# Performance work log

Hardware: AMD Instinct MI355X
Metric: run time of the kernel (lower is better)

The kernel has to match this reference:

```python
import jax, jax.numpy as jnp
import numpy as np

# ---- static config (mirrors GaussianLSS __init__) ----
ORF_H, ORF_W = 256, 704
FC, FH, FW = 128, 32, 88
D_ST, D_END, D_STEP = 4.0, 45.0, 1.0
OUT_C = 128
ERROR_TOL = 1.0
OPACITY_THR = 0.05
XB = (-50.0, 50.0, 1.0)
YB = (-50.0, 50.0, 1.0)
BEV_H = int(round((YB[1] - YB[0]) / YB[2]))
BEV_W = int(round((XB[1] - XB[0]) / XB[2]))
DS = np.arange(D_ST, D_END, D_STEP, dtype=np.float32)
D = DS.shape[0]  # 41
BN_EPS = 1e-3
CHUNK = 512      # gaussians composited per scan step (16896 = 33*512)
B, NCAM = 1, 6


def make_frustum():
    ds = jnp.broadcast_to(jnp.asarray(DS)[:, None, None], (D, FH, FW))
    xs = jnp.broadcast_to(jnp.linspace(0.0, ORF_W - 1.0, FW)[None, None, :], (D, FH, FW))
    ys = jnp.broadcast_to(jnp.linspace(0.0, ORF_H - 1.0, FH)[None, :, None], (D, FH, FW))
    return jnp.stack([xs, ys, ds], -1)  # [D,FH,FW,3]


def get_geometry(rots, trans, intrins, post_rots, post_trans):
    fr = make_frustum()
    pts = fr[None, None] - post_trans[:, :, None, None, None, :]
    pts = jnp.einsum('bnij,bndhwj->bndhwi', jnp.linalg.inv(post_rots), pts)
    pts = jnp.concatenate([pts[..., :2] * pts[..., 2:3], pts[..., 2:3]], -1)
    comb = jnp.einsum('bnij,bnjk->bnik', rots, jnp.linalg.inv(intrins))
    pts = jnp.einsum('bnij,bndhwj->bndhwi', comb, pts) + trans[:, :, None, None, None, :]
    return pts  # [B,N,D,FH,FW,3] ego-frame frustum points


def conv2d(x, w, b, pad):
    y = jax.lax.conv_general_dilated(x, w, (1, 1), [(pad, pad), (pad, pad)],
                                     dimension_numbers=('NCHW', 'OIHW', 'NCHW'))
    return y + b[None, :, None, None]


def bnorm(x, g, bt, m, v):
    s = (g / jnp.sqrt(v + BN_EPS))[None, :, None, None]
    return (x - m[None, :, None, None]) * s + bt[None, :, None, None]


def splat(means, cov6, colors, ops, valid_in):
    # Differentiable BEV gaussian rasterization (3DGS math, orthographic BEV camera,
    # all depths equal -> compositing in stable gaussian-index order).
    H, W = BEV_H, BEV_W
    sh, sw = H / 2.0, W / 2.0  # h/h_meters with FoV=2 (BEVCamera)
    my = -sh * means[:, 1] + H / 2.0  # pixel row (full_proj_transform row 0)
    mx = -sw * means[:, 0] + W / 2.0  # pixel col (row 1)
    a = sh * sh * cov6[:, 3] + 0.3    # 2D cov = J Sigma_xy J^T, +0.3 low-pass as in 3DGS
    c = sw * sw * cov6[:, 0] + 0.3
    b = sh * sw * cov6[:, 1]
    det = a * c - b * b
    valid = valid_in & (det > 0)
    inv_det = jnp.where(det > 0, 1.0 / det, 0.0)
    cA, cB, cC = c * inv_det, -b * inv_det, a * inv_det
    pi = jnp.repeat(jnp.arange(H, dtype=jnp.float32), W)  # [P] pixel rows
    pj = jnp.tile(jnp.arange(W, dtype=jnp.float32), H)    # [P] pixel cols
    G = means.shape[0]
    nchunk = G // CHUNK
    resh = lambda x: x.reshape((nchunk, CHUNK) + x.shape[1:])
    chunks = (resh(my), resh(mx), resh(cA), resh(cB), resh(cC),
              resh(ops), resh(valid), resh(colors))

    def body(carry, ch):
        logT, acc = carry
        my_c, mx_c, A, Bc, Cc, op_c, val_c, col_c = ch
        dI = pi[None, :] - my_c[:, None]                     # [Gc,P]
        dJ = pj[None, :] - mx_c[:, None]
        q = A[:, None] * dI * dI + 2.0 * Bc[:, None] * dI * dJ + Cc[:, None] * dJ * dJ
        alpha = jnp.minimum(0.99, op_c[:, None] * jnp.exp(-0.5 * q))
        alpha = jnp.where(val_c[:, None] & (q >= 0) & (alpha >= 1.0 / 255.0), alpha, 0.0)
        log1m = jnp.log1p(-alpha)
        cum = jnp.cumsum(log1m, axis=0)
        T = jnp.exp(logT[None, :] + cum - log1m)             # transmittance before each gaussian
        acc = acc + jnp.einsum('gp,gc->pc', alpha * T, col_c)
        return (logT + cum[-1], acc), None

    P = H * W
    init = (jnp.zeros((P,), jnp.float32), jnp.zeros((P, colors.shape[1]), jnp.float32))
    (_, acc), _ = jax.lax.scan(jax.checkpoint(body), init, chunks)
    return acc.reshape(H, W, -1).transpose(2, 0, 1)  # [C,H,W], bg is zeros


def _forward(cam2ego_rot, cam2ego_trans, cam_intrins, post_cam2ego_rot, post_cam2ego_trans,
             img_feats, conv1_w, conv1_b, bn1_g, bn1_b, bn1_m, bn1_v,
             conv2_w, conv2_b, bn2_g, bn2_b, bn2_m, bn2_v, conv3_w, conv3_b):
    geom = get_geometry(cam2ego_rot, cam2ego_trans, cam_intrins, post_cam2ego_rot, post_cam2ego_trans)
    b, n = img_feats.shape[:2]
    x = img_feats.reshape(b * n, FC, FH, FW)
    x = jax.nn.relu(bnorm(conv2d(x, conv1_w, conv1_b, 1), bn1_g, bn1_b, bn1_m, bn1_v))
    x = jax.nn.relu(bnorm(conv2d(x, conv2_w, conv2_b, 1), bn2_g, bn2_b, bn2_m, bn2_v))
    x = conv2d(x, conv3_w, conv3_b, 0)
    depth_prob = jax.nn.softmax(x[:, :D], axis=1).reshape(b, n, D, FH, FW)
    opac = jax.nn.sigmoid(x[:, D:D + 1]).reshape(b, n, FH, FW)
    feats = x[:, D + 1:].reshape(b, n, OUT_C, FH, FW)
    # per-pixel gaussian moments of the depth distribution (compute_gaussian)
    means = jnp.einsum('bndhw,bndhwi->bnhwi', depth_prob, geom)
    delta = means[:, :, None] - geom                                       # [B,N,D,FH,FW,3]
    cov = jnp.einsum('bndhw,bndhwi,bndhwj->bnhwij', depth_prob, delta, delta) * (ERROR_TOL ** 2 / 9.0)
    center = jnp.array([(XB[0] + XB[1]) / 2.0, (YB[0] + YB[1]) / 2.0, 0.0], jnp.float32)
    scale = jnp.array([2.0 / (XB[1] - XB[0]), 2.0 / (YB[1] - YB[0]), 1.0], jnp.float32)
    m_n = (means - center) * scale
    cov_n = cov * (scale[:, None] * scale[None, :])
    cov6 = jnp.stack([cov_n[..., 0, 0], cov_n[..., 0, 1], cov_n[..., 0, 2],
                      cov_n[..., 1, 1], cov_n[..., 1, 2], cov_n[..., 2, 2]], -1)
    g = n * FH * FW
    colors = feats.transpose(0, 1, 3, 4, 2).reshape(b, g, OUT_C)
    m_n = m_n.reshape(b, g, 3)
    cov6 = cov6.reshape(b, g, 6)
    ops = opac.reshape(b, g)
    mask = ops > OPACITY_THR  # opacity filtering == zero contribution, order preserved
    bev = jax.vmap(splat)(m_n, cov6, colors, ops, mask)                    # [B,C,H,W]
    num_gaussians = mask.astype(jnp.float32).sum(-1).mean()
    return bev, num_gaussians


def setup_inputs():
    key = jax.random.key(0)
    ks = jax.random.split(key, 8)
    # camera-to-ego rotations: cam->ego axis permutation composed with per-camera yaw
    yaw = np.linspace(0.0, 2.0 * np.pi, NCAM, endpoint=False).astype(np.float32)
    cz, sz = np.cos(yaw), np.sin(yaw)
    rotz = np.zeros((NCAM, 3, 3), np.float32)
    rotz[:, 0, 0] = cz; rotz[:, 0, 1] = -sz
    rotz[:, 1, 0] = sz; rotz[:, 1, 1] = cz
    rotz[:, 2, 2] = 1.0
    perm = np.array([[0.0, 0.0, 1.0], [-1.0, 0.0, 0.0], [0.0, -1.0, 0.0]], np.float32)
    rots = np.einsum('nij,jk->nik', rotz, perm)
    cam2ego_rot = jnp.asarray(np.broadcast_to(rots, (B, NCAM, 3, 3)).copy())
    cam2ego_trans = jax.random.normal(ks[0], (B, NCAM, 3), jnp.float32)
    K = np.array([[600.0, 0.0, ORF_W / 2.0], [0.0, 600.0, ORF_H / 2.0], [0.0, 0.0, 1.0]], np.float32)
    cam_intrins = jnp.asarray(np.broadcast_to(K, (B, NCAM, 3, 3)).copy())
    post_cam2ego_rot = jnp.broadcast_to(jnp.eye(3, dtype=jnp.float32), (B, NCAM, 3, 3)) + jnp.zeros((B, NCAM, 3, 3), jnp.float32)
    post_cam2ego_trans = jnp.zeros((B, NCAM, 3), jnp.float32)
    img_feats = jax.random.normal(ks[1], (B, NCAM, FC, FH, FW), jnp.float32)
    def conv_init(k, o, i, kh, kw):
        return jax.random.normal(k, (o, i, kh, kw), jnp.float32) * (1.0 / np.sqrt(i * kh * kw))
    return dict(cam2ego_rot=cam2ego_rot, cam2ego_trans=cam2ego_trans, cam_intrins=cam_intrins,
                post_cam2ego_rot=post_cam2ego_rot, post_cam2ego_trans=post_cam2ego_trans,
                img_feats=img_feats,
                conv1_w=conv_init(ks[2], FC, FC, 3, 3), conv1_b=jnp.zeros((FC,), jnp.float32),
                bn1_g=jnp.ones((FC,), jnp.float32), bn1_b=jnp.zeros((FC,), jnp.float32),
                bn1_m=jnp.zeros((FC,), jnp.float32), bn1_v=jnp.ones((FC,), jnp.float32),
                conv2_w=conv_init(ks[3], FC, FC, 3, 3), conv2_b=jnp.zeros((FC,), jnp.float32),
                bn2_g=jnp.ones((FC,), jnp.float32), bn2_b=jnp.zeros((FC,), jnp.float32),
                bn2_m=jnp.zeros((FC,), jnp.float32), bn2_v=jnp.ones((FC,), jnp.float32),
                conv3_w=conv_init(ks[4], OUT_C + D + 1, FC, 1, 1),
                conv3_b=jax.random.normal(ks[5], (OUT_C + D + 1,), jnp.float32) * 0.1)


def reference(cam2ego_rot, cam2ego_trans, cam_intrins, post_cam2ego_rot, post_cam2ego_trans,
              img_feats, conv1_w, conv1_b, bn1_g, bn1_b, bn1_m, bn1_v,
              conv2_w, conv2_b, bn2_g, bn2_b, bn2_m, bn2_v, conv3_w, conv3_b):
    return _forward(cam2ego_rot, cam2ego_trans, cam_intrins, post_cam2ego_rot, post_cam2ego_trans,
                    img_feats, conv1_w, conv1_b, bn1_g, bn1_b, bn1_m, bn1_v,
                    conv2_w, conv2_b, bn2_g, bn2_b, bn2_m, bn2_v, conv3_w, conv3_b)
```

## Files before the change

### kernel.cpp

```cpp
#include <hip/hip_runtime.h>

#define NCAM 6
#define FC   128
#define FH_  32
#define FW_  88
#define NPIX (FH_*FW_)
#define PH   34
#define PW   92
#define PPIX (PH*PW)
#define ND   41
#define X3D  42
#define OUTC 128
#define GTOT (NCAM*NPIX)
#define BEVH 100
#define BEVW 100
#define NPXB (BEVH*BEVW)
#define NTILE 25
#define NWORD 264
#define NMASKW (NTILE*NTILE*NWORD)
#define WCAP  70000
#define CSIZE 64
#define CBLK  2048

#define SZA     (NCAM*FC*PPIX)
#define WS_CAM  0
#define WS_A    256
#define WS_RB   (WS_A  + SZA)
#define WS_X3   (WS_RB + SZA)
#define WS_GS   (WS_X3 + NCAM*X3D*NPIX)
#define WS_WL   (WS_GS + GTOT*8)
#define WS_BASE (WS_WL + WCAP)

__device__ inline void inv3x3(const float* m, float* o) {
    float a=m[0],b=m[1],c=m[2],d=m[3],e=m[4],f=m[5],g=m[6],h=m[7],i=m[8];
    float A=e*i-f*h, B=c*h-b*i, C=b*f-c*e;
    float Dd=f*g-d*i, E=a*i-c*g, F=c*d-a*f;
    float Gg=d*h-e*g, H=b*g-a*h, I=a*e-b*d;
    float r = 1.0f/(a*A + b*Dd + c*Gg);
    o[0]=A*r; o[1]=B*r; o[2]=C*r; o[3]=Dd*r; o[4]=E*r; o[5]=F*r;
    o[6]=Gg*r; o[7]=H*r; o[8]=I*r;
}

__global__ __launch_bounds__(256) void pad_input_kernel(const float* __restrict__ src,
        float* __restrict__ dst, float* __restrict__ rb,
        float* __restrict__ outp, unsigned long long* __restrict__ masks) {
    int idx = blockIdx.x*256 + threadIdx.x;
    if (idx < NMASKW) masks[idx] = 0ull;
    if (idx <= NPXB*OUTC) outp[idx] = 0.0f;
    if (idx >= NCAM*FC*PPIX) return;
    int plane = idx / PPIX, pp = idx - plane*PPIX;
    int y = pp / PW, x = pp - y*PW;
    bool interior = (y >= 1 && y <= FH_ && x >= 1 && x <= FW_);
    float v = 0.0f;
    if (interior)
        v = src[(size_t)plane*NPIX + (y-1)*FW_ + (x-1)];
    dst[idx] = v;
    if (!interior) rb[idx] = 0.0f;
}

__global__ __launch_bounds__(128) void conv3x3_pf_kernel(
        const float* __restrict__ in, float* __restrict__ out, const float* __restrict__ w,
        const float* __restrict__ cb, const float* __restrict__ bg, const float* __restrict__ bb,
        const float* __restrict__ bm, const float* __restrict__ bv) {
    const int n   = blockIdx.x;
    const int co0 = blockIdx.y * 4;
    const int qid = blockIdx.z * 128 + threadIdx.x;
    if (qid >= 704) return;
    const int y = qid / 22, x0 = (qid - y*22) * 4;
    float scale[4], shift[4];
    #pragma unroll
    for (int c=0;c<4;c++) {
        float s = bg[co0+c] * rsqrtf(bv[co0+c] + 1e-3f);
        scale[c] = s;
        shift[c] = (cb[co0+c] - bm[co0+c]) * s + bb[co0+c];
    }
    float acc[4][4] = {};
    const float* ip = in + (size_t)n*FC*PPIX + y*PW + x0;
    const float* wb = w + (size_t)co0*FC*9;
    float4 p4[3]; float2 p2[3];
    #pragma unroll
    for (int r=0;r<3;r++) {
        p4[r] = *(const float4*)(ip + r*PW);
        p2[r] = *(const float2*)(ip + r*PW + 4);
    }
    for (int ci=0; ci<FC; ++ci) {
        float v[3][6];
        #pragma unroll
        for (int r=0;r<3;r++) {
            v[r][0]=p4[r].x; v[r][1]=p4[r].y; v[r][2]=p4[r].z; v[r][3]=p4[r].w;
            v[r][4]=p2[r].x; v[r][5]=p2[r].y;
        }
        if (ci + 1 < FC) {
            const float* ipn = ip + PPIX;
            #pragma unroll
            for (int r=0;r<3;r++) {
                p4[r] = *(const float4*)(ipn + r*PW);
                p2[r] = *(const float2*)(ipn + r*PW + 4);
            }
        }
        #pragma unroll
        for (int c=0;c<4;c++) {
            const float* wr = wb + (size_t)c*FC*9 + ci*9;
            float w00=wr[0],w01=wr[1],w02=wr[2],w10=wr[3],w11=wr[4],
                  w12=wr[5],w20=wr[6],w21=wr[7],w22=wr[8];
            #pragma unroll
            for (int p=0;p<4;p++) {
                float a = acc[c][p];
                a = fmaf(w00, v[0][p], a); a = fmaf(w01, v[0][p+1], a); a = fmaf(w02, v[0][p+2], a);
                a = fmaf(w10, v[1][p], a); a = fmaf(w11, v[1][p+1], a); a = fmaf(w12, v[1][p+2], a);
                a = fmaf(w20, v[2][p], a); a = fmaf(w21, v[2][p+1], a); a = fmaf(w22, v[2][p+2], a);
                acc[c][p] = a;
            }
        }
        ip += PPIX;
    }
    const int po = (y+1)*PW + (x0+1);
    #pragma unroll
    for (int c=0;c<4;c++) {
        float* op = out + ((size_t)n*FC + co0 + c)*PPIX + po;
        #pragma unroll
        for (int p=0;p<4;p++)
            op[p] = fmaxf(fmaf(acc[c][p], scale[c], shift[c]), 0.0f);
    }
}

__global__ __launch_bounds__(256) void conv1x1_kernel(const float* __restrict__ in,
        float* __restrict__ x3d, float* __restrict__ colors,
        const float* __restrict__ w, const float* __restrict__ b) {
    const int n   = blockIdx.x;
    const int px  = blockIdx.y * 256 + threadIdx.x;
    const int co0 = blockIdx.z * 8;
    const int y   = px / FW_, x = px - y*FW_;
    const int pp  = (y+1)*PW + (x+1);
    const float* wr[8];
    float acc[8];
    #pragma unroll
    for (int k=0;k<8;k++) {
        int co = min(co0 + k, 169);
        wr[k]  = w + (size_t)co*FC;
        acc[k] = b[co];
    }
    const float* ip = in + (size_t)n*FC*PPIX + pp;
    #pragma unroll 4
    for (int ci=0; ci<FC; ++ci) {
        float v = ip[(size_t)ci*PPIX];
        #pragma unroll
        for (int k=0;k<8;k++) acc[k] = fmaf(wr[k][ci], v, acc[k]);
    }
    #pragma unroll
    for (int k=0;k<8;k++) {
        int co = co0 + k;
        if (co < X3D)
            x3d[((size_t)n*X3D + co)*NPIX + px] = acc[k];
        else if (co < 170)
            colors[(((size_t)(n*NPIX + px)) << 7) + (co - X3D)] = acc[k];
    }
}

__global__ __launch_bounds__(256) void moments_masks_kernel(const float* __restrict__ x3,
        const float* __restrict__ rot, const float* __restrict__ tr,
        const float* __restrict__ intr, const float* __restrict__ prot,
        const float* __restrict__ ptr_, float* __restrict__ gauss,
        unsigned long long* __restrict__ masks, float* __restrict__ ng) {
    __shared__ float cc[24];
    const int n = blockIdx.x / 11;
    if (threadIdx.x == 0) {
        float M1[9], Ki[9];
        inv3x3(prot + n*9, M1);
        inv3x3(intr + n*9, Ki);
        const float* R = rot + n*9;
        #pragma unroll
        for (int i=0;i<9;i++) cc[i] = M1[i];
        #pragma unroll
        for (int i=0;i<3;i++) cc[9+i] = ptr_[n*3+i];
        #pragma unroll
        for (int i=0;i<3;i++)
            #pragma unroll
            for (int j=0;j<3;j++)
                cc[12+i*3+j] = R[i*3+0]*Ki[0+j] + R[i*3+1]*Ki[3+j] + R[i*3+2]*Ki[6+j];
        #pragma unroll
        for (int i=0;i<3;i++) cc[21+i] = tr[n*3+i];
    }
    __syncthreads();
    const int gi = blockIdx.x*256 + threadIdx.x;
    const int p  = gi - n*NPIX;
    const int h  = p / FW_, xp = p - h*FW_;
    float u = xp * (703.0f/87.0f);
    float v = h  * (255.0f/31.0f);
    float fx = u - cc[9], fy = v - cc[10], fz = -cc[11];
    float p0x = cc[0]*fx + cc[1]*fy + cc[2]*fz;
    float p0y = cc[3]*fx + cc[4]*fy + cc[5]*fz;
    float p0z = cc[6]*fx + cc[7]*fy + cc[8]*fz;
    const float* lg = x3 + (size_t)n*X3D*NPIX + p;

    float lgv[ND];
    #pragma unroll
    for (int d=0; d<ND; ++d) lgv[d] = lg[(size_t)d*NPIX];

    float mxl = -1e30f;
    #pragma unroll
    for (int d=0; d<ND; ++d) mxl = fmaxf(mxl, lgv[d]);

    float s=0.f, sgx=0.f, sgy=0.f;
    #pragma unroll
    for (int d=0; d<ND; ++d) {
        float e  = __expf(lgv[d] - mxl);
        lgv[d] = e;
        float dz = 4.0f + (float)d;
        float pz = p0z + dz*cc[8];
        float px = (p0x + dz*cc[2]) * pz;
        float py = (p0y + dz*cc[5]) * pz;
        float gx = cc[12]*px + cc[13]*py + cc[14]*pz + cc[21];
        float gy = cc[15]*px + cc[16]*py + cc[17]*pz + cc[22];
        s += e; sgx += e*gx; sgy += e*gy;
    }
    float inv_s = 1.0f/s;
    float mex = sgx*inv_s, mey = sgy*inv_s;
    float cxx=0.f, cxy=0.f, cyy=0.f;
    #pragma unroll
    for (int d=0; d<ND; ++d) {
        float e  = lgv[d];
        float dz = 4.0f + (float)d;
        float pz = p0z + dz*cc[8];
        float px = (p0x + dz*cc[2]) * pz;
        float py = (p0y + dz*cc[5]) * pz;
        float gx = cc[12]*px + cc[13]*py + cc[14]*pz + cc[21];
        float gy = cc[15]*px + cc[16]*py + cc[17]*pz + cc[22];
        float dxv = gx - mex, dyv = gy - mey;
        cxx += e*dxv*dxv; cxy += e*dxv*dyv; cyy += e*dyv*dyv;
    }
    const float k9 = inv_s * (1.0f/9.0f);
    cxx *= k9; cxy *= k9; cyy *= k9;

    float lo = lg[(size_t)ND*NPIX];
    float op = 1.0f/(1.0f + __expf(-lo));
    bool mask = op > 0.05f;

    const float SC = 0.02f, SH = 50.0f, SW = 50.0f;
    float my = -SH*(mey*SC) + 50.0f;
    float mx = -SW*(mex*SC) + 50.0f;
    float a  = SH*SH*(cyy*SC*SC) + 0.3f;
    float b  = SH*SW*(cxy*SC*SC);
    float c  = SW*SW*(cxx*SC*SC) + 0.3f;
    float det = a*c - b*b;
    bool valid = mask && (det > 0.0f);
    float A, B2, C, qm, ri, rj;
    if (valid) {
        float idet = 1.0f/det;
        A = c*idet; B2 = -2.0f*b*idet; C = a*idet;
        qm = 2.0f*__logf(255.0f*op);
        ri = sqrtf(qm*a); rj = sqrtf(qm*c);
    } else { A=B2=C=0.f; qm=-1.0f; ri=-1e30f; rj=-1e30f; }
    float* gp = gauss + (size_t)gi*8;
    gp[0]=my; gp[1]=mx; gp[2]=A; gp[3]=B2; gp[4]=C; gp[5]=qm; gp[6]=ri; gp[7]=rj;

    unsigned long long bal = __ballot(mask);
    if ((threadIdx.x & 63) == 0) atomicAdd(ng, (float)__popcll(bal));

    if (!valid) return;
    const float B = 0.5f*B2;
    const float invC = 1.0f / C;
    const float k2 = C*A - B*B;
    int ti0 = max(0, (int)floorf((my - ri) * 0.25f));
    int ti1 = min(NTILE-1, (int)floorf((my + ri) * 0.25f));
    const int wi = gi >> 6;
    const unsigned long long bit = 1ull << (gi & 63);
    for (int ti = ti0; ti <= ti1; ++ti) {
        float jmn = 1e30f, jmx = -1e30f;
        #pragma unroll
        for (int r = 0; r < 4; ++r) {
            int i = 4*ti + r;
            if (i < 0 || i > 99) continue;
            float di = (float)i - my;
            float disc = C*qm - k2*di*di;
            if (disc < 0.0f) continue;
            float sd = sqrtf(disc);
            float jc = -B*di;
            jmn = fminf(jmn, (jc - sd)*invC + mx);
            jmx = fmaxf(jmx, (jc + sd)*invC + mx);
        }
        if (jmx < jmn) continue;
        int jl = max(0, (int)ceilf(jmn));
        int jh = min(99, (int)floorf(jmx));
        if (jl > jh) continue;
        for (int tj = (jl >> 2); tj <= (jh >> 2); ++tj)
            atomicOr(&masks[(size_t)(ti*NTILE + tj)*NWORD + wi], bit);
    }
}

__global__ __launch_bounds__(256) void cnt_kernel(const unsigned long long* __restrict__ masks,
                                                  int* __restrict__ cnt) {
    __shared__ int sc;
    const int tile = blockIdx.x, t = threadIdx.x;
    if (t == 0) sc = 0;
    __syncthreads();
    if (t < NWORD) atomicAdd(&sc, __popcll(masks[(size_t)tile*NWORD + t]));
    __syncthreads();
    if (t == 0) cnt[tile] = sc;
}

__global__ __launch_bounds__(640) void scan_kernel(const int* __restrict__ cnt,
        int* __restrict__ off, int* __restrict__ choff, int* __restrict__ nwork) {
    __shared__ int wsum[16], wsum2[16];
    const int t = threadIdx.x;
    const int lane = t & 63, wv = t >> 6;
    int c  = (t < NTILE*NTILE) ? cnt[t] : 0;
    int ch = (c + CSIZE-1) >> 6;
    int v = c, v2 = ch;
    #pragma unroll
    for (int o = 1; o < 64; o <<= 1) {
        int u  = __shfl_up(v,  (unsigned)o, 64);
        int u2 = __shfl_up(v2, (unsigned)o, 64);
        if (lane >= o) { v += u; v2 += u2; }
    }
    if (lane == 63) { wsum[wv] = v; wsum2[wv] = v2; }
    __syncthreads();
    int pre = 0, pre2 = 0;
    for (int w2 = 0; w2 < wv; ++w2) { pre += wsum[w2]; pre2 += wsum2[w2]; }
    int inc = v + pre, inc2 = v2 + pre2;
    if (t < NTILE*NTILE) { off[t] = inc - c; choff[t] = inc2 - ch; }
    if (t == NTILE*NTILE - 1) {
        off[NTILE*NTILE] = inc;
        choff[NTILE*NTILE] = inc2;
        nwork[0] = (inc2 > WCAP) ? WCAP : inc2;
    }
}

__global__ __launch_bounds__(256) void fill_kernel(const unsigned long long* __restrict__ masks,
        const int* __restrict__ cnt, const int* __restrict__ off, const int* __restrict__ choff,
        unsigned short* __restrict__ list, int* __restrict__ wl) {
    __shared__ unsigned long long sw[NWORD];
    __shared__ int wpre[NWORD];
    const int tile = blockIdx.x, t = threadIdx.x;
    if (t < NWORD) sw[t] = masks[(size_t)tile*NWORD + t];
    __syncthreads();
    if (t == 0) {
        int run = 0;
        for (int w2 = 0; w2 < NWORD; ++w2) { wpre[w2] = run; run += __popcll(sw[w2]); }
    }
    __syncthreads();
    if (t < NWORD) {
        unsigned long long m = sw[t];
        int pos = off[tile] + wpre[t], base = t << 6;
        while (m) { int b = __builtin_ctzll(m); m &= m - 1; list[pos++] = (unsigned short)(base + b); }
    }
    int nch = (cnt[tile] + CSIZE-1)/CSIZE;
    int c0 = choff[tile];
    if (t < nch && c0 + t < WCAP) wl[c0 + t] = (tile << 9) | t;
}

__device__ inline float eval_alpha(const float4 g0, const float4 g1, float fi, float fj) {
    float dI = fi - g0.x, dJ = fj - g0.y;
    float q = dI*(g0.z*dI + g0.w*dJ) + g1.x*dJ*dJ;
    if (q < 0.0f || q > g1.y) return 0.0f;
    return fminf(0.99f, 0.003921568627f * __expf(0.5f*(g1.y - q)));
}

__global__ __launch_bounds__(256) void chunk_sums_kernel(const float* __restrict__ gauss,
        const unsigned short* __restrict__ list, const int* __restrict__ cnt,
        const int* __restrict__ off, const int* __restrict__ wl, const int* __restrict__ nwork,
        float* __restrict__ base) {
    const int nw = nwork[0];
    const int lane = threadIdx.x & 63;
    const int wid  = (blockIdx.x * 256 + threadIdx.x) >> 6;
    const int nwv  = (gridDim.x * 256) >> 6;
    const int px = lane & 15, kg = lane >> 4;
    for (int e = wid; e < nw; e += nwv) {
        int v = wl[e], tile = v >> 9, c = v & 511;
        int hbase = off[tile] + (c << 6);
        int nh = min(CSIZE, cnt[tile] - (c << 6));
        const int i0 = (tile / NTILE) * 4, j0 = (tile % NTILE) * 4;
        const float fi = (float)(i0 + (px >> 2)), fj = (float)(j0 + (px & 3));
        float s = 1.0f;
        for (int k = kg; k < nh; k += 4) {
            int g = list[hbase + k];
            float4 g0 = *(const float4*)(gauss + ((size_t)g << 3));
            float4 g1 = *(const float4*)(gauss + ((size_t)g << 3) + 4);
            float a = eval_alpha(g0, g1, fi, fj);
            s *= (1.0f - a);
        }
        s *= __shfl_xor(s, 16, 64);
        s *= __shfl_xor(s, 32, 64);
        if (lane < 16) base[(size_t)e*16 + lane] = s;
    }
}

__global__ __launch_bounds__(256) void chunk_prefix_kernel(const int* __restrict__ choff,
                                                           float* __restrict__ base) {
    __shared__ float part[16][17];
    const int tile = blockIdx.x, t = threadIdx.x;
    const int c0 = choff[tile], nch = choff[tile+1] - c0;
    if (nch == 0) return;
    const int px = t & 15, cg = t >> 4;
    const int L16 = (nch + 15) >> 4;
    const int a0 = cg*L16, a1 = min(nch, a0 + L16);
    float s = 1.0f;
    for (int c = a0; c < a1; ++c) s *= base[(size_t)(c0 + c)*16 + px];
    part[cg][px] = s;
    __syncthreads();
    if (t < 16) {
        float run = 1.0f;
        #pragma unroll
        for (int k = 0; k < 16; ++k) { float tmp = part[k][t]; part[k][t] = run; run *= tmp; }
    }
    __syncthreads();
    float run = part[cg][px];
    for (int c = a0; c < a1; ++c) {
        size_t idx = (size_t)(c0 + c)*16 + px;
        float tmp = base[idx];
        base[idx] = run;
        run *= tmp;
    }
}

__global__ __launch_bounds__(256) void composite_kernel(const float* __restrict__ gauss,
        const float* __restrict__ colors, const unsigned short* __restrict__ list,
        const int* __restrict__ cnt, const int* __restrict__ off, const int* __restrict__ wl,
        const int* __restrict__ nwork, const float* __restrict__ base, float* __restrict__ out) {
    const int nw = nwork[0];
    const int t = threadIdx.x;
    const int lane = t & 63;
    const int e_px = t >> 4, e_kg = t & 15;
    const int a_cs4 = t & 31, a_pxq = t >> 5;
    __shared__ unsigned short slist[2][CSIZE];
    __shared__ float s_w[CSIZE][17];
    const int per = (nw + CBLK - 1) / CBLK;
    int e0 = blockIdx.x * per;
    if (e0 >= nw) return;
    int e1 = min(nw, e0 + per);

    float4 acc0 = make_float4(0.f,0.f,0.f,0.f);
    float4 acc1 = make_float4(0.f,0.f,0.f,0.f);
    int cur_tile = wl[e0] >> 9;
    int cur_i0 = (cur_tile / NTILE) * 4, cur_j0 = (cur_tile % NTILE) * 4;

    int buf = 0;
    {
        int v = wl[e0], tl = v >> 9, c = v & 511;
        int nh0 = min(CSIZE, cnt[tl] - (c << 6));
        if (t < nh0) slist[0][t] = list[off[tl] + (c << 6) + t];
    }

    for (int e = e0; e < e1; ++e) {
        int v = wl[e], tile = v >> 9, c = v & 511;
        if (tile != cur_tile) {
            const int pix0 = (cur_i0 + (a_pxq >> 2)) * BEVW + cur_j0 + (a_pxq & 3);
            const int pix1 = pix0 + 2 * BEVW;
            float* op = out + (size_t)(a_cs4 << 2) * NPXB;
            atomicAdd(op + 0*NPXB + pix0, acc0.x); atomicAdd(op + 1*NPXB + pix0, acc0.y);
            atomicAdd(op + 2*NPXB + pix0, acc0.z); atomicAdd(op + 3*NPXB + pix0, acc0.w);
            atomicAdd(op + 0*NPXB + pix1, acc1.x); atomicAdd(op + 1*NPXB + pix1, acc1.y);
            atomicAdd(op + 2*NPXB + pix1, acc1.z); atomicAdd(op + 3*NPXB + pix1, acc1.w);
            acc0 = make_float4(0.f,0.f,0.f,0.f);
            acc1 = make_float4(0.f,0.f,0.f,0.f);
            cur_tile = tile;
            cur_i0 = (tile / NTILE) * 4; cur_j0 = (tile % NTILE) * 4;
        }
        const int nh = min(CSIZE, cnt[cur_tile] - (c << 6));
        __syncthreads();
        if (e + 1 < e1) {
            int v2 = wl[e+1], tl2 = v2 >> 9, c2 = v2 & 511;
            int nh2 = min(CSIZE, cnt[tl2] - (c2 << 6));
            if (t < nh2) slist[buf^1][t] = list[off[tl2] + (c2 << 6) + t];
        }
        {
            const float fi = (float)(cur_i0 + (e_px >> 2)), fj = (float)(cur_j0 + (e_px & 3));
            const int k0 = e_kg << 2;
            float a4[4]; float p = 1.0f;
            #pragma unroll
            for (int i = 0; i < 4; ++i) {
                int k = k0 + i;
                float a = 0.0f;
                if (k < nh) {
                    int g = slist[buf][k];
                    float4 g0 = *(const float4*)(gauss + ((size_t)g << 3));
                    float4 g1 = *(const float4*)(gauss + ((size_t)g << 3) + 4);
                    a = eval_alpha(g0, g1, fi, fj);
                }
                a4[i] = a;
                p *= (1.0f - a);
            }
            float s = p;
            #pragma unroll
            for (int o = 1; o < 16; o <<= 1) {
                float u = __shfl_up(s, (unsigned)o, 64);
                if ((lane & 15) >= o) s *= u;
            }
            float ex = __shfl_up(s, 1u, 64);
            float T = base[(size_t)e*16 + e_px] * (((lane & 15) == 0) ? 1.0f : ex);
            #pragma unroll
            for (int i = 0; i < 4; ++i) {
                float wv = a4[i] * T; T -= wv;
                s_w[k0 + i][e_px] = wv;
            }
        }
        __syncthreads();
        const float* colbase = colors;
        if (nh == CSIZE) {
            #pragma unroll 8
            for (int k = 0; k < CSIZE; ++k) {
                int g = slist[buf][k];
                float w0 = s_w[k][a_pxq];
                float w1 = s_w[k][a_pxq + 8];
                float4 cl = *(const float4*)(colbase + ((size_t)g << 7) + (a_cs4 << 2));
                acc0.x = fmaf(w0, cl.x, acc0.x); acc0.y = fmaf(w0, cl.y, acc0.y);
                acc0.z = fmaf(w0, cl.z, acc0.z); acc0.w = fmaf(w0, cl.w, acc0.w);
                acc1.x = fmaf(w1, cl.x, acc1.x); acc1.y = fmaf(w1, cl.y, acc1.y);
                acc1.z = fmaf(w1, cl.z, acc1.z); acc1.w = fmaf(w1, cl.w, acc1.w);
            }
        } else {
            #pragma unroll 4
            for (int k = 0; k < nh; ++k) {
                int g = slist[buf][k];
                float w0 = s_w[k][a_pxq];
                float w1 = s_w[k][a_pxq + 8];
                float4 cl = *(const float4*)(colbase + ((size_t)g << 7) + (a_cs4 << 2));
                acc0.x = fmaf(w0, cl.x, acc0.x); acc0.y = fmaf(w0, cl.y, acc0.y);
                acc0.z = fmaf(w0, cl.z, acc0.z); acc0.w = fmaf(w0, cl.w, acc0.w);
                acc1.x = fmaf(w1, cl.x, acc1.x); acc1.y = fmaf(w1, cl.y, acc1.y);
                acc1.z = fmaf(w1, cl.z, acc1.z); acc1.w = fmaf(w1, cl.w, acc1.w);
            }
        }
        buf ^= 1;
    }
    const int pix0 = (cur_i0 + (a_pxq >> 2)) * BEVW + cur_j0 + (a_pxq & 3);
    const int pix1 = pix0 + 2 * BEVW;
    float* op = out + (size_t)(a_cs4 << 2) * NPXB;
    atomicAdd(op + 0*NPXB + pix0, acc0.x); atomicAdd(op + 1*NPXB + pix0, acc0.y);
    atomicAdd(op + 2*NPXB + pix0, acc0.z); atomicAdd(op + 3*NPXB + pix0, acc0.w);
    atomicAdd(op + 0*NPXB + pix1, acc1.x); atomicAdd(op + 1*NPXB + pix1, acc1.y);
    atomicAdd(op + 2*NPXB + pix1, acc1.z); atomicAdd(op + 3*NPXB + pix1, acc1.w);
}

extern "C" void kernel_launch(void* const* d_in, const int* in_sizes, int n_in,
                              void* d_out, int out_size, void* d_ws, size_t ws_size,
                              hipStream_t stream) {
    const float* rot  = (const float*)d_in[0];
    const float* tr   = (const float*)d_in[1];
    const float* intr = (const float*)d_in[2];
    const float* prot = (const float*)d_in[3];
    const float* ptr_ = (const float*)d_in[4];
    const float* img  = (const float*)d_in[5];
    const float* c1w  = (const float*)d_in[6];  const float* c1b = (const float*)d_in[7];
    const float* b1g  = (const float*)d_in[8];  const float* b1b = (const float*)d_in[9];
    const float* b1m  = (const float*)d_in[10]; const float* b1v = (const float*)d_in[11];
    const float* c2w  = (const float*)d_in[12]; const float* c2b = (const float*)d_in[13];
    const float* b2g  = (const float*)d_in[14]; const float* b2b = (const float*)d_in[15];
    const float* b2m  = (const float*)d_in[16]; const float* b2v = (const float*)d_in[17];
    const float* c3w  = (const float*)d_in[18]; const float* c3b = (const float*)d_in[19];
    float* out = (float*)d_out;
    float* ws  = (float*)d_ws;
    float* RA  = ws + WS_A;
    float* RB  = ws + WS_RB;
    float* X3B = ws + WS_X3;
    float* GS  = ws + WS_GS;
    int*   WL  = (int*)(ws + WS_WL);
    float* BASE = ws + WS_BASE;
    unsigned long long* MASKS = (unsigned long long*)BASE;
    int* AUXI = (int*)(ws + WS_X3 + 330000);
    int* CNT = AUXI;
    int* OFF = AUXI + 640;
    int* CHOFF = AUXI + 1280;
    int* NWORK = AUXI + 1920;
    unsigned short* LIST = (unsigned short*)RA;
    float* COL = RB;
    float* ngp = out + (size_t)NPXB*OUTC;

    pad_input_kernel<<<(NCAM*FC*PPIX + 255)/256, 256, 0, stream>>>(img, RA, RB, out, MASKS);
    conv3x3_pf_kernel<<<dim3(NCAM,32,6), 128, 0, stream>>>(RA, RB, c1w, c1b, b1g, b1b, b1m, b1v);
    conv3x3_pf_kernel<<<dim3(NCAM,32,6), 128, 0, stream>>>(RB, RA, c2w, c2b, b2g, b2b, b2m, b2v);
    conv1x1_kernel<<<dim3(NCAM,11,22), 256, 0, stream>>>(RA, X3B, COL, c3w, c3b);
    moments_masks_kernel<<<GTOT/256, 256, 0, stream>>>(X3B, rot, tr, intr, prot, ptr_,
                                                       GS, MASKS, ngp);
    cnt_kernel<<<NTILE*NTILE, 256, 0, stream>>>(MASKS, CNT);
    scan_kernel<<<1, 640, 0, stream>>>(CNT, OFF, CHOFF, NWORK);
    fill_kernel<<<NTILE*NTILE, 256, 0, stream>>>(MASKS, CNT, OFF, CHOFF, LIST, WL);
    chunk_sums_kernel<<<8192, 256, 0, stream>>>(GS, LIST, CNT, OFF, WL, NWORK, BASE);
    chunk_prefix_kernel<<<NTILE*NTILE, 256, 0, stream>>>(CHOFF, BASE);
    composite_kernel<<<CBLK, 256, 0, stream>>>(GS, COL, LIST, CNT, OFF, WL, NWORK, BASE, out);
}
```

Baseline: 473.2 us.

## Split gaussian chunk across wave halves with 4-pixel register tiles in composite

Reassigns composite threads so each handles one channel quad for four pixels of a BEV row, with the two 32-lane halves of each wave taking even and odd gaussians of the chunk. This doubles reuse of each color float4 load across pixels and halves the per-thread loop trip count. A cross-half shuffle reduction before the atomic writes merges the partial sums, so each pixel still gets one atomic per channel. It costs more accumulator registers and adds shuffle work.

```diff
diff --git a/kernel.cpp b/kernel.cpp
--- a/kernel.cpp
+++ b/kernel.cpp
@@ -421,7 +421,9 @@
     const int t = threadIdx.x;
     const int lane = t & 63;
     const int e_px = t >> 4, e_kg = t & 15;
-    const int a_cs4 = t & 31, a_pxq = t >> 5;
+    const int cs4 = t & 31;
+    const int par = (t >> 5) & 1;
+    const int pq  = t >> 6;
     __shared__ unsigned short slist[2][CSIZE];
     __shared__ float s_w[CSIZE][17];
     const int per = (nw + CBLK - 1) / CBLK;
@@ -429,8 +431,9 @@
     if (e0 >= nw) return;
     int e1 = min(nw, e0 + per);
 
-    float4 acc0 = make_float4(0.f,0.f,0.f,0.f);
-    float4 acc1 = make_float4(0.f,0.f,0.f,0.f);
+    float4 acc[4];
+    #pragma unroll
+    for (int j=0;j<4;j++) acc[j] = make_float4(0.f,0.f,0.f,0.f);
     int cur_tile = wl[e0] >> 9;
     int cur_i0 = (cur_tile / NTILE) * 4, cur_j0 = (cur_tile % NTILE) * 4;
 
@@ -444,15 +447,25 @@
     for (int e = e0; e < e1; ++e) {
         int v = wl[e], tile = v >> 9, c = v & 511;
         if (tile != cur_tile) {
-            const int pix0 = (cur_i0 + (a_pxq >> 2)) * BEVW + cur_j0 + (a_pxq & 3);
-            const int pix1 = pix0 + 2 * BEVW;
-            float* op = out + (size_t)(a_cs4 << 2) * NPXB;
-            atomicAdd(op + 0*NPXB + pix0, acc0.x); atomicAdd(op + 1*NPXB + pix0, acc0.y);
-            atomicAdd(op + 2*NPXB + pix0, acc0.z); atomicAdd(op + 3*NPXB + pix0, acc0.w);
-            atomicAdd(op + 0*NPXB + pix1, acc1.x); atomicAdd(op + 1*NPXB + pix1, acc1.y);
-            atomicAdd(op + 2*NPXB + pix1, acc1.z); atomicAdd(op + 3*NPXB + pix1, acc1.w);
-            acc0 = make_float4(0.f,0.f,0.f,0.f);
-            acc1 = make_float4(0.f,0.f,0.f,0.f);
+            #pragma unroll
+            for (int j = 0; j < 4; ++j) {
+                acc[j].x += __shfl_xor(acc[j].x, 32, 64);
+                acc[j].y += __shfl_xor(acc[j].y, 32, 64);
+                acc[j].z += __shfl_xor(acc[j].z, 32, 64);
+                acc[j].w += __shfl_xor(acc[j].w, 32, 64);
+            }
+            if (par == 0) {
+                float* op = out + (size_t)(cs4 << 2) * NPXB + (cur_i0 + pq) * BEVW + cur_j0;
+                #pragma unroll
+                for (int j = 0; j < 4; ++j) {
+                    atomicAdd(op + 0*NPXB + j, acc[j].x);
+                    atomicAdd(op + 1*NPXB + j, acc[j].y);
+                    atomicAdd(op + 2*NPXB + j, acc[j].z);
+                    atomicAdd(op + 3*NPXB + j, acc[j].w);
+                }
+            }
+            #pragma unroll
+            for (int j=0;j<4;j++) acc[j] = make_float4(0.f,0.f,0.f,0.f);
             cur_tile = tile;
             cur_i0 = (tile / NTILE) * 4; cur_j0 = (tile % NTILE) * 4;
         }
@@ -495,41 +508,61 @@
             }
         }
         __syncthreads();
-        const float* colbase = colors;
         if (nh == CSIZE) {
             #pragma unroll 8
-            for (int k = 0; k < CSIZE; ++k) {
-                int g = slist[buf][k];
-                float w0 = s_w[k][a_pxq];
-                float w1 = s_w[k][a_pxq + 8];
-                float4 cl = *(const float4*)(colbase + ((size_t)g << 7) + (a_cs4 << 2));
-                acc0.x = fmaf(w0, cl.x, acc0.x); acc0.y = fmaf(w0, cl.y, acc0.y);
-                acc0.z = fmaf(w0, cl.z, acc0.z); acc0.w = fmaf(w0, cl.w, acc0.w);
-                acc1.x = fmaf(w1, cl.x, acc1.x); acc1.y = fmaf(w1, cl.y, acc1.y);
-                acc1.z = fmaf(w1, cl.z, acc1.z); acc1.w = fmaf(w1, cl.w, acc1.w);
+            for (int k = 0; k < CSIZE/2; ++k) {
+                const int idx = (k << 1) | par;
+                int g = slist[buf][idx];
+                const float* swr = s_w[idx] + (pq << 2);
+                float w0 = swr[0], w1 = swr[1], w2 = swr[2], w3 = swr[3];
+                float4 cl = *(const float4*)(colors + ((size_t)g << 7) + (cs4 << 2));
+                acc[0].x = fmaf(w0, cl.x, acc[0].x); acc[0].y = fmaf(w0, cl.y, acc[0].y);
+                acc[0].z = fmaf(w0, cl.z, acc[0].z); acc[0].w = fmaf(w0, cl.w, acc[0].w);
+                acc[1].x = fmaf(w1, cl.x, acc[1].x); acc[1].y = fmaf(w1, cl.y, acc[1].y);
+                acc[1].z = fmaf(w1, cl.z, acc[1].z); acc[1].w = fmaf(w1, cl.w, acc[1].w);
+                acc[2].x = fmaf(w2, cl.x, acc[2].x); acc[2].y = fmaf(w2, cl.y, acc[2].y);
+                acc[2].z = fmaf(w2, cl.z, acc[2].z); acc[2].w = fmaf(w2, cl.w, acc[2].w);
+                acc[3].x = fmaf(w3, cl.x, acc[3].x); acc[3].y = fmaf(w3, cl.y, acc[3].y);
+                acc[3].z = fmaf(w3, cl.z, acc[3].z); acc[3].w = fmaf(w3, cl.w, acc[3].w);
             }
         } else {
             #pragma unroll 4
-            for (int k = 0; k < nh; ++k) {
-                int g = slist[buf][k];
-                float w0 = s_w[k][a_pxq];
-                float w1 = s_w[k][a_pxq + 8];
-                float4 cl = *(const float4*)(colbase + ((size_t)g << 7) + (a_cs4 << 2));
-                acc0.x = fmaf(w0, cl.x, acc0.x); acc0.y = fmaf(w0, cl.y, acc0.y);
-                acc0.z = fmaf(w0, cl.z, acc0.z); acc0.w = fmaf(w0, cl.w, acc0.w);
-                acc1.x = fmaf(w1, cl.x, acc1.x); acc1.y = fmaf(w1, cl.y, acc1.y);
-                acc1.z = fmaf(w1, cl.z, acc1.z); acc1.w = fmaf(w1, cl.w, acc1.w);
+            for (int k = 0; k < CSIZE/2; ++k) {
+                const int idx = (k << 1) | par;
+                if (idx >= nh) break;
+                int g = slist[buf][idx];
+                const float* swr = s_w[idx] + (pq << 2);
+                float w0 = swr[0], w1 = swr[1], w2 = swr[2], w3 = swr[3];
+                float4 cl = *(const float4*)(colors + ((size_t)g << 7) + (cs4 << 2));
+                acc[0].x = fmaf(w0, cl.x, acc[0].x); acc[0].y = fmaf(w0, cl.y, acc[0].y);
+                acc[0].z = fmaf(w0, cl.z, acc[0].z); acc[0].w = fmaf(w0, cl.w, acc[0].w);
+                acc[1].x = fmaf(w1, cl.x, acc[1].x); acc[1].y = fmaf(w1, cl.y, acc[1].y);
+                acc[1].z = fmaf(w1, cl.z, acc[1].z); acc[1].w = fmaf(w1, cl.w, acc[1].w);
+                acc[2].x = fmaf(w2, cl.x, acc[2].x); acc[2].y = fmaf(w2, cl.y, acc[2].y);
+                acc[2].z = fmaf(w2, cl.z, acc[2].z); acc[2].w = fmaf(w2, cl.w, acc[2].w);
+                acc[3].x = fmaf(w3, cl.x, acc[3].x); acc[3].y = fmaf(w3, cl.y, acc[3].y);
+                acc[3].z = fmaf(w3, cl.z, acc[3].z); acc[3].w = fmaf(w3, cl.w, acc[3].w);
             }
         }
         buf ^= 1;
     }
-    const int pix0 = (cur_i0 + (a_pxq >> 2)) * BEVW + cur_j0 + (a_pxq & 3);
-    const int pix1 = pix0 + 2 * BEVW;
-    float* op = out + (size_t)(a_cs4 << 2) * NPXB;
-    atomicAdd(op + 0*NPXB + pix0, acc0.x); atomicAdd(op + 1*NPXB + pix0, acc0.y);
-    atomicAdd(op + 2*NPXB + pix0, acc0.z); atomicAdd(op + 3*NPXB + pix0, acc0.w);
-    atomicAdd(op + 0*NPXB + pix1, acc1.x); atomicAdd(op + 1*NPXB + pix1, acc1.y);
-    atomicAdd(op + 2*NPXB + pix1, acc1.z); atomicAdd(op + 3*NPXB + pix1, acc1.w);
+    #pragma unroll
+    for (int j = 0; j < 4; ++j) {
+        acc[j].x += __shfl_xor(acc[j].x, 32, 64);
+        acc[j].y += __shfl_xor(acc[j].y, 32, 64);
+        acc[j].z += __shfl_xor(acc[j].z, 32, 64);
+        acc[j].w += __shfl_xor(acc[j].w, 32, 64);
+    }
+    if (par == 0) {
+        float* op = out + (size_t)(cs4 << 2) * NPXB + (cur_i0 + pq) * BEVW + cur_j0;
+        #pragma unroll
+        for (int j = 0; j < 4; ++j) {
+            atomicAdd(op + 0*NPXB + j, acc[j].x);
+            atomicAdd(op + 1*NPXB + j, acc[j].y);
+            atomicAdd(op + 2*NPXB + j, acc[j].z);
+            atomicAdd(op + 3*NPXB + j, acc[j].w);
+        }
+    }
 }
 
 extern "C" void kernel_launch(void* const* d_in, const int* in_sizes, int n_in,
```

New measurement: 559.7 us. +18.3%, slower.
